# Kernel tuning notes

Measured on AMD Instinct MI355X. Metric: run time of the kernel, lower is better.

The kernel has to match this reference:

```python
import jax, jax.numpy as jnp
import numpy as np

N = 50000
E = 1600000
D_IN = 256
HID = 64
HEADS = 4


def setup_inputs() -> dict:
    key = jax.random.key(0)
    ks = jax.random.split(key, 8)
    x = jax.random.normal(ks[0], (N, D_IN), dtype=jnp.float32)
    edge_index = jax.random.randint(ks[1], (2, E), 0, N, dtype=jnp.int32)
    # GATConv params (PyG default: concat=True, negative_slope=0.2, add_self_loops=True)
    W = jax.random.normal(ks[2], (D_IN, HEADS * HID), dtype=jnp.float32) * (1.0 / np.sqrt(D_IN))
    att_src = jax.random.normal(ks[3], (HEADS, HID), dtype=jnp.float32) * 0.1
    att_dst = jax.random.normal(ks[4], (HEADS, HID), dtype=jnp.float32) * 0.1
    bias = jnp.zeros((HEADS * HID,), dtype=jnp.float32)
    # fc1: Linear(hidden*4, 3)
    fc1_W = jax.random.normal(ks[5], (HEADS * HID, 3), dtype=jnp.float32) * (1.0 / np.sqrt(HEADS * HID))
    fc1_b = jnp.zeros((3,), dtype=jnp.float32)
    return {"x": x, "edge_index": edge_index, "W": W, "att_src": att_src,
            "att_dst": att_dst, "bias": bias, "fc1_W": fc1_W, "fc1_b": fc1_b}


def _gat_conv(x, edge_index, W, att_src, att_dst, bias):
    n = x.shape[0]
    xp = (x @ W).reshape(n, HEADS, HID)  # [N,H,C]
    # add self loops (PyG default)
    loops = jnp.arange(n, dtype=edge_index.dtype)
    src = jnp.concatenate([edge_index[0], loops])  # [E+N]
    dst = jnp.concatenate([edge_index[1], loops])
    a_src = jnp.sum(xp * att_src, axis=-1)  # [N,H]
    a_dst = jnp.sum(xp * att_dst, axis=-1)
    alpha = jax.nn.leaky_relu(a_src[src] + a_dst[dst], negative_slope=0.2)  # [E+N,H]
    # segment softmax over incoming edges of each dst node
    amax = jax.ops.segment_max(alpha, dst, num_segments=n)
    ex = jnp.exp(alpha - amax[dst])
    denom = jax.ops.segment_sum(ex, dst, num_segments=n)
    alpha = ex / (denom[dst] + 1e-16)
    msg = xp[src] * alpha[:, :, None]  # [E+N,H,C]
    out = jax.ops.segment_sum(msg, dst, num_segments=n)  # [N,H,C]
    return out.reshape(n, HEADS * HID) + bias


def reference(x, edge_index, W, att_src, att_dst, bias, fc1_W, fc1_b):
    # dropout is identity at inference
    h = _gat_conv(x, edge_index, W, att_src, att_dst, bias)
    h = jax.nn.leaky_relu(h, negative_slope=0.01)  # F.leaky_relu default slope
    edge_rep = h[edge_index[0]] * h[edge_index[1]] * 0.5  # [E, H*HID]
    edge_scores = edge_rep @ fc1_W + fc1_b  # [E, 3]
    return edge_scores
```

## Files before the change

### kernel.cpp

```cpp
#include <hip/hip_runtime.h>
#include <hip/hip_fp16.h>
#include <math.h>

constexpr int N    = 50000;
constexpr int E    = 1600000;
constexpr int F    = 256;
constexpr int EL   = E + N;
constexpr int NBLK = (N + 255) / 256;

typedef _Float16 v8hf __attribute__((ext_vector_type(8)));
typedef float    v4f  __attribute__((ext_vector_type(4)));

__global__ void k_cvt_x(const float* __restrict__ x, _Float16* __restrict__ xh) {
  const size_t i = ((size_t)blockIdx.x * 256 + threadIdx.x) * 4;
  const float4 v = *(const float4*)(x + i);
  _Float16 h[4] = {(_Float16)v.x, (_Float16)v.y, (_Float16)v.z, (_Float16)v.w};
  *(uint2*)(xh + i) = *(const uint2*)h;
}

__global__ void k_cvt_w(const float* __restrict__ W, _Float16* __restrict__ wt) {
  const int id = blockIdx.x * 256 + threadIdx.x;
  const int n = id >> 8, k = id & 255;
  wt[id] = (_Float16)W[k * 256 + n];
}

__global__ void k_cvt_w3(const float* __restrict__ fc1W, _Float16* __restrict__ wt3h) {
  const int id = blockIdx.x * 256 + threadIdx.x;
  const int n = id >> 8, k = id & 255;
  wt3h[id] = (n < 3) ? (_Float16)(0.5f * fc1W[k * 3 + n]) : (_Float16)0.f;
}

__global__ __launch_bounds__(256) void k_xw_mfma(
    const _Float16* __restrict__ xh, const _Float16* __restrict__ wt,
    const float* __restrict__ att_src, const float* __restrict__ att_dst,
    __half* __restrict__ xp, float* __restrict__ a_src, float* __restrict__ a_dst) {
  const int wv   = threadIdx.x >> 6;
  const int lane = threadIdx.x & 63;
  const int q = lane >> 4, l16 = lane & 15;
  const int m0 = blockIdx.x * 16;
  const int c0 = wv * 64;

  v4f acc[4] = {{0,0,0,0},{0,0,0,0},{0,0,0,0},{0,0,0,0}};
  const _Float16* arow = xh + (size_t)(m0 + l16) * 256 + q * 8;
  const _Float16* brow = wt + (size_t)(c0 + l16) * 256 + q * 8;

  for (int kc = 0; kc < 256; kc += 32) {
    const v8hf a = *(const v8hf*)(arow + kc);
    #pragma unroll
    for (int tn = 0; tn < 4; ++tn) {
      const v8hf b = *(const v8hf*)(brow + (size_t)tn * 16 * 256 + kc);
      acc[tn] = __builtin_amdgcn_mfma_f32_16x16x32_f16(a, b, acc[tn], 0, 0, 0);
    }
  }

  #pragma unroll
  for (int tn = 0; tn < 4; ++tn) {
    const int col = c0 + tn * 16 + l16;
    #pragma unroll
    for (int r = 0; r < 4; ++r)
      xp[(size_t)(m0 + q * 4 + r) * 256 + col] = __float2half_rn(acc[tn][r]);
  }

  float aw[4], dw[4];
  #pragma unroll
  for (int tn = 0; tn < 4; ++tn) {
    aw[tn] = att_src[c0 + tn * 16 + l16];
    dw[tn] = att_dst[c0 + tn * 16 + l16];
  }
  #pragma unroll
  for (int r = 0; r < 4; ++r) {
    float ps = acc[0][r]*aw[0] + acc[1][r]*aw[1] + acc[2][r]*aw[2] + acc[3][r]*aw[3];
    float pd = acc[0][r]*dw[0] + acc[1][r]*dw[1] + acc[2][r]*dw[2] + acc[3][r]*dw[3];
    #pragma unroll
    for (int off = 1; off < 16; off <<= 1) {
      ps += __shfl_xor(ps, off, 16);
      pd += __shfl_xor(pd, off, 16);
    }
    if (l16 == 0) {
      a_src[(m0 + q * 4 + r) * 4 + wv] = ps;
      a_dst[(m0 + q * 4 + r) * 4 + wv] = pd;
    }
  }
}

__global__ void k_hist(const int* __restrict__ ei, int* __restrict__ counts) {
  const int i = blockIdx.x * blockDim.x + threadIdx.x;
  if (i < E) atomicAdd(&counts[ei[E + i]], 1);
}

__global__ __launch_bounds__(256) void k_scan1(
    const int* __restrict__ counts, int* __restrict__ offsets, int* __restrict__ partials) {
  __shared__ int s[256];
  const int t = threadIdx.x;
  const int i = blockIdx.x * 256 + t;
  const int v = (i < N) ? counts[i] + 1 : 0;
  s[t] = v;
  __syncthreads();
  for (int off = 1; off < 256; off <<= 1) {
    const int add = (t >= off) ? s[t - off] : 0;
    __syncthreads();
    s[t] += add;
    __syncthreads();
  }
  if (i < N) offsets[i] = s[t] - v;
  if (t == 255) partials[blockIdx.x] = s[255];
}

__global__ __launch_bounds__(256) void k_scan2(int* __restrict__ partials) {
  __shared__ int s[256];
  const int t = threadIdx.x;
  const int v = (t < NBLK) ? partials[t] : 0;
  s[t] = v;
  __syncthreads();
  for (int off = 1; off < 256; off <<= 1) {
    const int add = (t >= off) ? s[t - off] : 0;
    __syncthreads();
    s[t] += add;
    __syncthreads();
  }
  if (t < NBLK) partials[t] = s[t] - v;
}

__global__ void k_scan3(int* __restrict__ offsets, const int* __restrict__ partials,
                        int* __restrict__ cursor) {
  const int i = blockIdx.x * 256 + threadIdx.x;
  if (i < N) {
    const int v = offsets[i] + partials[blockIdx.x];
    offsets[i] = v;
    cursor[i]  = v;
  }
  if (i == 0) offsets[N] = EL;
}

__global__ void k_scatter(const int* __restrict__ ei, int* __restrict__ cursor,
                          int2* __restrict__ se) {
  const int i = blockIdx.x * blockDim.x + threadIdx.x;
  if (i >= EL) return;
  int s, d, id;
  if (i < E) { s = ei[i]; d = ei[E + i]; id = i; }
  else       { s = d = i - E; id = -1; }
  const int pos = atomicAdd(&cursor[d], 1);
  se[pos] = make_int2(s, id);
}

__global__ __launch_bounds__(128) void k_agg(
    const __half* __restrict__ xp, const float* __restrict__ a_src,
    const float* __restrict__ a_dst, const int2* __restrict__ se,
    const int* __restrict__ offsets, const float* __restrict__ bias,
    __half* __restrict__ h) {
  const int n = blockIdx.x * 2 + (threadIdx.x >> 6);
  const int lane = threadIdx.x & 63;
  const int hd = lane >> 4, es = lane & 15;
  const int beg = offsets[n], end = offsets[n + 1];
  const float adst = a_dst[n * 4 + hd];
  const __half* xb = xp + (size_t)lane * 4;

  float a0 = 0.f, a1 = 0.f, a2 = 0.f, a3 = 0.f, den = 0.f;

  for (int c = beg; c < end; c += 16) {
    const int cnt = min(16, end - c);
    int sv = 0; float wvv = 0.f;
    if (es < cnt) {
      sv = se[c + es].x;
      float al = a_src[sv * 4 + hd] + adst;
      al = al > 0.f ? al : 0.2f * al;
      wvv = __expf(al);
    }
    int j = 0;
    for (; j + 4 <= cnt; j += 4) {
      const int   s0 = __shfl(sv, j + 0, 16), s1 = __shfl(sv, j + 1, 16);
      const int   s2 = __shfl(sv, j + 2, 16), s3 = __shfl(sv, j + 3, 16);
      const float w0 = __shfl(wvv, j + 0, 16), w1 = __shfl(wvv, j + 1, 16);
      const float w2 = __shfl(wvv, j + 2, 16), w3 = __shfl(wvv, j + 3, 16);
      const uint2 r0 = *(const uint2*)(xb + (size_t)s0 * 256);
      const uint2 r1 = *(const uint2*)(xb + (size_t)s1 * 256);
      const uint2 r2 = *(const uint2*)(xb + (size_t)s2 * 256);
      const uint2 r3 = *(const uint2*)(xb + (size_t)s3 * 256);
      den += (w0 + w1) + (w2 + w3);
      {
        const __half2* p = (const __half2*)&r0;
        const float2 lo = __half22float2(p[0]), hi = __half22float2(p[1]);
        a0 += w0 * lo.x; a1 += w0 * lo.y; a2 += w0 * hi.x; a3 += w0 * hi.y;
      }
      {
        const __half2* p = (const __half2*)&r1;
        const float2 lo = __half22float2(p[0]), hi = __half22float2(p[1]);
        a0 += w1 * lo.x; a1 += w1 * lo.y; a2 += w1 * hi.x; a3 += w1 * hi.y;
      }
      {
        const __half2* p = (const __half2*)&r2;
        const float2 lo = __half22float2(p[0]), hi = __half22float2(p[1]);
        a0 += w2 * lo.x; a1 += w2 * lo.y; a2 += w2 * hi.x; a3 += w2 * hi.y;
      }
      {
        const __half2* p = (const __half2*)&r3;
        const float2 lo = __half22float2(p[0]), hi = __half22float2(p[1]);
        a0 += w3 * lo.x; a1 += w3 * lo.y; a2 += w3 * hi.x; a3 += w3 * hi.y;
      }
    }
    for (; j < cnt; ++j) {
      const int   s = __shfl(sv, j, 16);
      const float w = __shfl(wvv, j, 16);
      const uint2 r = *(const uint2*)(xb + (size_t)s * 256);
      const __half2* p = (const __half2*)&r;
      const float2 lo = __half22float2(p[0]), hi = __half22float2(p[1]);
      den += w;
      a0 += w * lo.x; a1 += w * lo.y; a2 += w * hi.x; a3 += w * hi.y;
    }
  }

  const float inv = 1.f / (den + 1e-16f);
  const float4 bv = *(const float4*)(bias + lane * 4);
  float o0 = a0 * inv + bv.x, o1 = a1 * inv + bv.y;
  float o2 = a2 * inv + bv.z, o3 = a3 * inv + bv.w;
  o0 = o0 > 0.f ? o0 : 0.01f * o0;
  o1 = o1 > 0.f ? o1 : 0.01f * o1;
  o2 = o2 > 0.f ? o2 : 0.01f * o2;
  o3 = o3 > 0.f ? o3 : 0.01f * o3;
  const __half2 p0 = __floats2half2_rn(o0, o1), p1 = __floats2half2_rn(o2, o3);
  uint2 st;
  st.x = *(const unsigned*)&p0;
  st.y = *(const unsigned*)&p1;
  *(uint2*)(h + (size_t)n * 256 + lane * 4) = st;
}

__global__ __launch_bounds__(256) void k_score_mfma(
    const _Float16* __restrict__ h, const int2* __restrict__ se,
    const int* __restrict__ offsets, const _Float16* __restrict__ wt3h,
    const float* __restrict__ fc1b, float* __restrict__ out) {
  const int n = blockIdx.x * 4 + (threadIdx.x >> 6);
  const int lane = threadIdx.x & 63;
  const int q = lane >> 4, l16 = lane & 15;

  v8hf bfrag[8];
  {
    const _Float16* brow = wt3h + l16 * 256 + q * 8;
    #pragma unroll
    for (int kci = 0; kci < 8; ++kci)
      bfrag[kci] = *(const v8hf*)(brow + kci * 32);
  }
  v8hf hdv[8];
  {
    const _Float16* drow = h + (size_t)n * 256 + q * 8;
    #pragma unroll
    for (int kci = 0; kci < 8; ++kci)
      hdv[kci] = *(const v8hf*)(drow + kci * 32);
  }
  const float bn = (l16 < 3) ? fc1b[l16] : 0.f;

  const int beg = offsets[n], end = offsets[n + 1];
  for (int c = beg; c < end; c += 16) {
    const int idx = c + l16;
    int s = -1, eid = -1;
    if (idx < end) { const int2 p = se[idx]; s = p.x; eid = p.y; }

    v8hf av[8] = {};
    if (s >= 0) {
      const _Float16* srow = h + (size_t)s * 256 + q * 8;
      #pragma unroll
      for (int kci = 0; kci < 8; ++kci)
        av[kci] = *(const v8hf*)(srow + kci * 32);
    }

    v4f acc = {0.f, 0.f, 0.f, 0.f};
    #pragma unroll
    for (int kci = 0; kci < 8; ++kci) {
      const v8hf ar = av[kci] * hdv[kci];
      acc = __builtin_amdgcn_mfma_f32_16x16x32_f16(ar, bfrag[kci], acc, 0, 0, 0);
    }

    #pragma unroll
    for (int r = 0; r < 4; ++r) {
      const int m = q * 4 + r;
      const int em = __shfl(eid, m, 16);
      if (l16 < 3 && c + m < end && em >= 0)
        out[(size_t)em * 3 + l16] = acc[r] + bn;
    }
  }
}

static inline size_t align256(size_t b) { return (b + 255) & ~(size_t)255; }

extern "C" void kernel_launch(void* const* d_in, const int* in_sizes, int n_in,
                              void* d_out, int out_size, void* d_ws, size_t ws_size,
                              hipStream_t stream) {
  const float* x    = (const float*)d_in[0];
  const int*   ei   = (const int*)  d_in[1];
  const float* W    = (const float*)d_in[2];
  const float* attS = (const float*)d_in[3];
  const float* attD = (const float*)d_in[4];
  const float* bias = (const float*)d_in[5];
  const float* fc1W = (const float*)d_in[6];
  const float* fc1b = (const float*)d_in[7];
  float*       out  = (float*)d_out;
  char*        ws   = (char*)d_ws;

  size_t off = 0;
  auto alloc = [&](size_t bytes) -> void* {
    void* p = ws + off;
    off += align256(bytes);
    return p;
  };
  _Float16* xh     = (_Float16*)alloc((size_t)N * F * sizeof(_Float16));
  _Float16* wt     = (_Float16*)alloc((size_t)F * F * sizeof(_Float16));
  _Float16* wt3h   = (_Float16*)alloc((size_t)16 * F * sizeof(_Float16));
  __half*   xp     = (__half*)  alloc((size_t)N * F * sizeof(__half));
  __half*   hbuf   = (__half*)  alloc((size_t)N * F * sizeof(__half));
  float*    a_src  = (float*)   alloc((size_t)N * 4 * sizeof(float));
  float*    a_dst  = (float*)   alloc((size_t)N * 4 * sizeof(float));
  int*      counts = (int*)     alloc((size_t)N * sizeof(int));
  int*      offs   = (int*)     alloc((size_t)(N + 1) * sizeof(int));
  int*      partial= (int*)     alloc(256 * sizeof(int));
  int*      cursor = (int*)     alloc((size_t)N * sizeof(int));
  int2*     se     = (int2*)    alloc((size_t)EL * sizeof(int2));

  hipMemsetAsync(counts, 0, (size_t)N * sizeof(int), stream);

  k_cvt_x<<<(N * F / 4 + 255) / 256, 256, 0, stream>>>(x, xh);
  k_cvt_w<<<F * F / 256, 256, 0, stream>>>(W, wt);
  k_cvt_w3<<<16, 256, 0, stream>>>(fc1W, wt3h);
  k_xw_mfma<<<N / 16, 256, 0, stream>>>(xh, wt, attS, attD, xp, a_src, a_dst);
  k_hist<<<(E + 255) / 256, 256, 0, stream>>>(ei, counts);
  k_scan1<<<NBLK, 256, 0, stream>>>(counts, offs, partial);
  k_scan2<<<1, 256, 0, stream>>>(partial);
  k_scan3<<<NBLK, 256, 0, stream>>>(offs, partial, cursor);
  k_scatter<<<(EL + 255) / 256, 256, 0, stream>>>(ei, cursor, se);
  k_agg<<<N / 2, 128, 0, stream>>>(xp, a_src, a_dst, se, offs, bias, hbuf);
  k_score_mfma<<<(N + 3) / 4, 256, 0, stream>>>((const _Float16*)hbuf, se, offs,
                                                wt3h, fc1b, out);
}
```

Before: 665.0 us.

## Fuse prep kernels, fold x conversion and histogram into GEMM, flatten scoring

The separate x, W and fc1 conversion kernels and the memset are merged into one prep kernel. The fp32 x is now converted to half inside the MFMA GEMM, and the degree histogram runs as a tail loop of that GEMM. The scan's second and third passes are merged. Aggregation now uses two waves per node, each taking alternating 16-edge chunks, with the partial sums reduced through shared memory. Scoring becomes a flat grid-stride loop over 16-edge chunks and reads the destination index from a widened int4 CSR entry. The aim is fewer launches, no materialised half copy of x, and better load balance for high-degree nodes, at the cost of doubling the CSR size and redundant dst-row gathers in scoring.

```diff
diff --git a/kernel.cpp b/kernel.cpp
--- a/kernel.cpp
+++ b/kernel.cpp
@@ -7,32 +7,31 @@
 constexpr int F    = 256;
 constexpr int EL   = E + N;
 constexpr int NBLK = (N + 255) / 256;
+constexpr int CH   = (EL + 15) / 16;
 
 typedef _Float16 v8hf __attribute__((ext_vector_type(8)));
 typedef float    v4f  __attribute__((ext_vector_type(4)));
 
-__global__ void k_cvt_x(const float* __restrict__ x, _Float16* __restrict__ xh) {
-  const size_t i = ((size_t)blockIdx.x * 256 + threadIdx.x) * 4;
-  const float4 v = *(const float4*)(x + i);
-  _Float16 h[4] = {(_Float16)v.x, (_Float16)v.y, (_Float16)v.z, (_Float16)v.w};
-  *(uint2*)(xh + i) = *(const uint2*)h;
-}
-
-__global__ void k_cvt_w(const float* __restrict__ W, _Float16* __restrict__ wt) {
-  const int id = blockIdx.x * 256 + threadIdx.x;
-  const int n = id >> 8, k = id & 255;
-  wt[id] = (_Float16)W[k * 256 + n];
-}
-
-__global__ void k_cvt_w3(const float* __restrict__ fc1W, _Float16* __restrict__ wt3h) {
-  const int id = blockIdx.x * 256 + threadIdx.x;
-  const int n = id >> 8, k = id & 255;
-  wt3h[id] = (n < 3) ? (_Float16)(0.5f * fc1W[k * 3 + n]) : (_Float16)0.f;
+__global__ __launch_bounds__(256) void k_prep(
+    const float* __restrict__ W, const float* __restrict__ fc1W,
+    _Float16* __restrict__ wt, _Float16* __restrict__ wt3h,
+    int* __restrict__ counts) {
+  const int t = blockIdx.x * 256 + threadIdx.x;
+  {
+    const int n = t >> 8, k = t & 255;
+    wt[t] = (_Float16)W[k * 256 + n];
+  }
+  if (t < 4096) {
+    const int n = t >> 8, k = t & 255;
+    wt3h[t] = (n < 3) ? (_Float16)(0.5f * fc1W[k * 3 + n]) : (_Float16)0.f;
+  }
+  if (t < N) counts[t] = 0;
 }
 
 __global__ __launch_bounds__(256) void k_xw_mfma(
-    const _Float16* __restrict__ xh, const _Float16* __restrict__ wt,
+    const float* __restrict__ x, const _Float16* __restrict__ wt,
     const float* __restrict__ att_src, const float* __restrict__ att_dst,
+    const int* __restrict__ ei, int* __restrict__ counts,
     __half* __restrict__ xp, float* __restrict__ a_src, float* __restrict__ a_dst) {
   const int wv   = threadIdx.x >> 6;
   const int lane = threadIdx.x & 63;
@@ -41,11 +40,14 @@
   const int c0 = wv * 64;
 
   v4f acc[4] = {{0,0,0,0},{0,0,0,0},{0,0,0,0},{0,0,0,0}};
-  const _Float16* arow = xh + (size_t)(m0 + l16) * 256 + q * 8;
+  const float*    arow = x  + (size_t)(m0 + l16) * 256 + q * 8;
   const _Float16* brow = wt + (size_t)(c0 + l16) * 256 + q * 8;
 
   for (int kc = 0; kc < 256; kc += 32) {
-    const v8hf a = *(const v8hf*)(arow + kc);
+    const float4 f0 = *(const float4*)(arow + kc);
+    const float4 f1 = *(const float4*)(arow + kc + 4);
+    const v8hf a = {(_Float16)f0.x, (_Float16)f0.y, (_Float16)f0.z, (_Float16)f0.w,
+                    (_Float16)f1.x, (_Float16)f1.y, (_Float16)f1.z, (_Float16)f1.w};
     #pragma unroll
     for (int tn = 0; tn < 4; ++tn) {
       const v8hf b = *(const v8hf*)(brow + (size_t)tn * 16 * 256 + kc);
@@ -81,11 +83,9 @@
       a_dst[(m0 + q * 4 + r) * 4 + wv] = pd;
     }
   }
-}
-
-__global__ void k_hist(const int* __restrict__ ei, int* __restrict__ counts) {
-  const int i = blockIdx.x * blockDim.x + threadIdx.x;
-  if (i < E) atomicAdd(&counts[ei[E + i]], 1);
+
+  const int gid = blockIdx.x * 256 + threadIdx.x;
+  for (int i = gid; i < E; i += 800000) atomicAdd(&counts[ei[E + i]], 1);
 }
 
 __global__ __launch_bounds__(256) void k_scan1(
@@ -106,9 +106,11 @@
   if (t == 255) partials[blockIdx.x] = s[255];
 }
 
-__global__ __launch_bounds__(256) void k_scan2(int* __restrict__ partials) {
+__global__ __launch_bounds__(256) void k_scan3b(
+    int* __restrict__ offsets, const int* __restrict__ partials,
+    int* __restrict__ cursor) {
   __shared__ int s[256];
-  const int t = threadIdx.x;
+  const int t = threadIdx.x, b = blockIdx.x;
   const int v = (t < NBLK) ? partials[t] : 0;
   s[t] = v;
   __syncthreads();
@@ -118,38 +120,35 @@
     s[t] += add;
     __syncthreads();
   }
-  if (t < NBLK) partials[t] = s[t] - v;
-}
-
-__global__ void k_scan3(int* __restrict__ offsets, const int* __restrict__ partials,
-                        int* __restrict__ cursor) {
-  const int i = blockIdx.x * 256 + threadIdx.x;
+  const int pre = (b == 0) ? 0 : s[b - 1];
+  const int i = b * 256 + t;
   if (i < N) {
-    const int v = offsets[i] + partials[blockIdx.x];
-    offsets[i] = v;
-    cursor[i]  = v;
+    const int val = offsets[i] + pre;
+    offsets[i] = val;
+    cursor[i]  = val;
   }
   if (i == 0) offsets[N] = EL;
 }
 
 __global__ void k_scatter(const int* __restrict__ ei, int* __restrict__ cursor,
-                          int2* __restrict__ se) {
+                          int4* __restrict__ se) {
   const int i = blockIdx.x * blockDim.x + threadIdx.x;
   if (i >= EL) return;
   int s, d, id;
   if (i < E) { s = ei[i]; d = ei[E + i]; id = i; }
   else       { s = d = i - E; id = -1; }
   const int pos = atomicAdd(&cursor[d], 1);
-  se[pos] = make_int2(s, id);
+  se[pos] = make_int4(s, id, d, 0);
 }
 
 __global__ __launch_bounds__(128) void k_agg(
     const __half* __restrict__ xp, const float* __restrict__ a_src,
-    const float* __restrict__ a_dst, const int2* __restrict__ se,
+    const float* __restrict__ a_dst, const int4* __restrict__ se,
     const int* __restrict__ offsets, const float* __restrict__ bias,
     __half* __restrict__ h) {
-  const int n = blockIdx.x * 2 + (threadIdx.x >> 6);
-  const int lane = threadIdx.x & 63;
+  const int n = blockIdx.x;
+  const int t = threadIdx.x;
+  const int wv = t >> 6, lane = t & 63;
   const int hd = lane >> 4, es = lane & 15;
   const int beg = offsets[n], end = offsets[n + 1];
   const float adst = a_dst[n * 4 + hd];
@@ -157,7 +156,7 @@
 
   float a0 = 0.f, a1 = 0.f, a2 = 0.f, a3 = 0.f, den = 0.f;
 
-  for (int c = beg; c < end; c += 16) {
+  for (int c = beg + wv * 16; c < end; c += 32) {
     const int cnt = min(16, end - c);
     int sv = 0; float wvv = 0.f;
     if (es < cnt) {
@@ -166,106 +165,100 @@
       al = al > 0.f ? al : 0.2f * al;
       wvv = __expf(al);
     }
-    int j = 0;
-    for (; j + 4 <= cnt; j += 4) {
-      const int   s0 = __shfl(sv, j + 0, 16), s1 = __shfl(sv, j + 1, 16);
-      const int   s2 = __shfl(sv, j + 2, 16), s3 = __shfl(sv, j + 3, 16);
-      const float w0 = __shfl(wvv, j + 0, 16), w1 = __shfl(wvv, j + 1, 16);
-      const float w2 = __shfl(wvv, j + 2, 16), w3 = __shfl(wvv, j + 3, 16);
-      const uint2 r0 = *(const uint2*)(xb + (size_t)s0 * 256);
-      const uint2 r1 = *(const uint2*)(xb + (size_t)s1 * 256);
-      const uint2 r2 = *(const uint2*)(xb + (size_t)s2 * 256);
-      const uint2 r3 = *(const uint2*)(xb + (size_t)s3 * 256);
-      den += (w0 + w1) + (w2 + w3);
-      {
-        const __half2* p = (const __half2*)&r0;
+    if (cnt == 16) {
+      #pragma unroll
+      for (int g = 0; g < 2; ++g) {
+        int ss[8]; float ww[8]; uint2 rr[8];
+        #pragma unroll
+        for (int j = 0; j < 8; ++j) {
+          ss[j] = __shfl(sv,  g * 8 + j, 16);
+          ww[j] = __shfl(wvv, g * 8 + j, 16);
+        }
+        #pragma unroll
+        for (int j = 0; j < 8; ++j) rr[j] = *(const uint2*)(xb + (size_t)ss[j] * 256);
+        #pragma unroll
+        for (int j = 0; j < 8; ++j) {
+          const __half2* p = (const __half2*)&rr[j];
+          const float2 lo = __half22float2(p[0]), hi = __half22float2(p[1]);
+          den += ww[j];
+          a0 += ww[j] * lo.x; a1 += ww[j] * lo.y;
+          a2 += ww[j] * hi.x; a3 += ww[j] * hi.y;
+        }
+      }
+    } else {
+      for (int j = 0; j < cnt; ++j) {
+        const int   s = __shfl(sv, j, 16);
+        const float w = __shfl(wvv, j, 16);
+        const uint2 r = *(const uint2*)(xb + (size_t)s * 256);
+        const __half2* p = (const __half2*)&r;
         const float2 lo = __half22float2(p[0]), hi = __half22float2(p[1]);
-        a0 += w0 * lo.x; a1 += w0 * lo.y; a2 += w0 * hi.x; a3 += w0 * hi.y;
+        den += w;
+        a0 += w * lo.x; a1 += w * lo.y; a2 += w * hi.x; a3 += w * hi.y;
       }
-      {
-        const __half2* p = (const __half2*)&r1;
-        const float2 lo = __half22float2(p[0]), hi = __half22float2(p[1]);
-        a0 += w1 * lo.x; a1 += w1 * lo.y; a2 += w1 * hi.x; a3 += w1 * hi.y;
-      }
-      {
-        const __half2* p = (const __half2*)&r2;
-        const float2 lo = __half22float2(p[0]), hi = __half22float2(p[1]);
-        a0 += w2 * lo.x; a1 += w2 * lo.y; a2 += w2 * hi.x; a3 += w2 * hi.y;
-      }
-      {
-        const __half2* p = (const __half2*)&r3;
-        const float2 lo = __half22float2(p[0]), hi = __half22float2(p[1]);
-        a0 += w3 * lo.x; a1 += w3 * lo.y; a2 += w3 * hi.x; a3 += w3 * hi.y;
-      }
-    }
-    for (; j < cnt; ++j) {
-      const int   s = __shfl(sv, j, 16);
-      const float w = __shfl(wvv, j, 16);
-      const uint2 r = *(const uint2*)(xb + (size_t)s * 256);
-      const __half2* p = (const __half2*)&r;
-      const float2 lo = __half22float2(p[0]), hi = __half22float2(p[1]);
-      den += w;
-      a0 += w * lo.x; a1 += w * lo.y; a2 += w * hi.x; a3 += w * hi.y;
-    }
-  }
-
-  const float inv = 1.f / (den + 1e-16f);
-  const float4 bv = *(const float4*)(bias + lane * 4);
-  float o0 = a0 * inv + bv.x, o1 = a1 * inv + bv.y;
-  float o2 = a2 * inv + bv.z, o3 = a3 * inv + bv.w;
-  o0 = o0 > 0.f ? o0 : 0.01f * o0;
-  o1 = o1 > 0.f ? o1 : 0.01f * o1;
-  o2 = o2 > 0.f ? o2 : 0.01f * o2;
-  o3 = o3 > 0.f ? o3 : 0.01f * o3;
-  const __half2 p0 = __floats2half2_rn(o0, o1), p1 = __floats2half2_rn(o2, o3);
-  uint2 st;
-  st.x = *(const unsigned*)&p0;
-  st.y = *(const unsigned*)&p1;
-  *(uint2*)(h + (size_t)n * 256 + lane * 4) = st;
-}
-
-__global__ __launch_bounds__(256) void k_score_mfma(
-    const _Float16* __restrict__ h, const int2* __restrict__ se,
-    const int* __restrict__ offsets, const _Float16* __restrict__ wt3h,
-    const float* __restrict__ fc1b, float* __restrict__ out) {
-  const int n = blockIdx.x * 4 + (threadIdx.x >> 6);
+    }
+  }
+
+  __shared__ float ra[256];
+  __shared__ float rd[64];
+  if (wv == 1) {
+    ra[lane * 4 + 0] = a0; ra[lane * 4 + 1] = a1;
+    ra[lane * 4 + 2] = a2; ra[lane * 4 + 3] = a3;
+    rd[lane] = den;
+  }
+  __syncthreads();
+  if (wv == 0) {
+    a0 += ra[lane * 4 + 0]; a1 += ra[lane * 4 + 1];
+    a2 += ra[lane * 4 + 2]; a3 += ra[lane * 4 + 3];
+    den += rd[lane];
+    const float inv = 1.f / (den + 1e-16f);
+    const float4 bv = *(const float4*)(bias + lane * 4);
+    float o0 = a0 * inv + bv.x, o1 = a1 * inv + bv.y;
+    float o2 = a2 * inv + bv.z, o3 = a3 * inv + bv.w;
+    o0 = o0 > 0.f ? o0 : 0.01f * o0;
+    o1 = o1 > 0.f ? o1 : 0.01f * o1;
+    o2 = o2 > 0.f ? o2 : 0.01f * o2;
+    o3 = o3 > 0.f ? o3 : 0.01f * o3;
+    const __half2 p0 = __floats2half2_rn(o0, o1), p1 = __floats2half2_rn(o2, o3);
+    uint2 st;
+    st.x = *(const unsigned*)&p0;
+    st.y = *(const unsigned*)&p1;
+    *(uint2*)(h + (size_t)n * 256 + lane * 4) = st;
+  }
+}
+
+__global__ __launch_bounds__(256) void k_score_flat(
+    const _Float16* __restrict__ h, const int4* __restrict__ se,
+    const _Float16* __restrict__ wt3h, const float* __restrict__ fc1b,
+    float* __restrict__ out, int total_waves) {
   const int lane = threadIdx.x & 63;
   const int q = lane >> 4, l16 = lane & 15;
+  const int wgid = blockIdx.x * 4 + (threadIdx.x >> 6);
 
   v8hf bfrag[8];
   {
     const _Float16* brow = wt3h + l16 * 256 + q * 8;
     #pragma unroll
-    for (int kci = 0; kci < 8; ++kci)
-      bfrag[kci] = *(const v8hf*)(brow + kci * 32);
-  }
-  v8hf hdv[8];
-  {
-    const _Float16* drow = h + (size_t)n * 256 + q * 8;
-    #pragma unroll
-    for (int kci = 0; kci < 8; ++kci)
-      hdv[kci] = *(const v8hf*)(drow + kci * 32);
+    for (int kci = 0; kci < 8; ++kci) bfrag[kci] = *(const v8hf*)(brow + kci * 32);
   }
   const float bn = (l16 < 3) ? fc1b[l16] : 0.f;
 
-  const int beg = offsets[n], end = offsets[n + 1];
-  for (int c = beg; c < end; c += 16) {
-    const int idx = c + l16;
-    int s = -1, eid = -1;
-    if (idx < end) { const int2 p = se[idx]; s = p.x; eid = p.y; }
-
-    v8hf av[8] = {};
-    if (s >= 0) {
-      const _Float16* srow = h + (size_t)s * 256 + q * 8;
-      #pragma unroll
-      for (int kci = 0; kci < 8; ++kci)
-        av[kci] = *(const v8hf*)(srow + kci * 32);
-    }
+  for (int ch = wgid; ch < CH; ch += total_waves) {
+    const int idx = ch * 16 + l16;
+    int s = 0, d = 0, eid = -1;
+    if (idx < EL) { const int4 p = se[idx]; s = p.x; eid = p.y; d = p.z; }
+
+    const _Float16* srow = h + (size_t)s * 256 + q * 8;
+    const _Float16* drow = h + (size_t)d * 256 + q * 8;
+    v8hf av[8], dv[8];
+    #pragma unroll
+    for (int kci = 0; kci < 8; ++kci) av[kci] = *(const v8hf*)(srow + kci * 32);
+    #pragma unroll
+    for (int kci = 0; kci < 8; ++kci) dv[kci] = *(const v8hf*)(drow + kci * 32);
 
     v4f acc = {0.f, 0.f, 0.f, 0.f};
     #pragma unroll
     for (int kci = 0; kci < 8; ++kci) {
-      const v8hf ar = av[kci] * hdv[kci];
+      const v8hf ar = av[kci] * dv[kci];
       acc = __builtin_amdgcn_mfma_f32_16x16x32_f16(ar, bfrag[kci], acc, 0, 0, 0);
     }
 
@@ -273,7 +266,7 @@
     for (int r = 0; r < 4; ++r) {
       const int m = q * 4 + r;
       const int em = __shfl(eid, m, 16);
-      if (l16 < 3 && c + m < end && em >= 0)
+      if (l16 < 3 && em >= 0)
         out[(size_t)em * 3 + l16] = acc[r] + bn;
     }
   }
@@ -301,7 +294,6 @@
     off += align256(bytes);
     return p;
   };
-  _Float16* xh     = (_Float16*)alloc((size_t)N * F * sizeof(_Float16));
   _Float16* wt     = (_Float16*)alloc((size_t)F * F * sizeof(_Float16));
   _Float16* wt3h   = (_Float16*)alloc((size_t)16 * F * sizeof(_Float16));
   __half*   xp     = (__half*)  alloc((size_t)N * F * sizeof(__half));
@@ -312,20 +304,16 @@
   int*      offs   = (int*)     alloc((size_t)(N + 1) * sizeof(int));
   int*      partial= (int*)     alloc(256 * sizeof(int));
   int*      cursor = (int*)     alloc((size_t)N * sizeof(int));
-  int2*     se     = (int2*)    alloc((size_t)EL * sizeof(int2));
-
-  hipMemsetAsync(counts, 0, (size_t)N * sizeof(int), stream);
-
-  k_cvt_x<<<(N * F / 4 + 255) / 256, 256, 0, stream>>>(x, xh);
-  k_cvt_w<<<F * F / 256, 256, 0, stream>>>(W, wt);
-  k_cvt_w3<<<16, 256, 0, stream>>>(fc1W, wt3h);
-  k_xw_mfma<<<N / 16, 256, 0, stream>>>(xh, wt, attS, attD, xp, a_src, a_dst);
-  k_hist<<<(E + 255) / 256, 256, 0, stream>>>(ei, counts);
+  int4*     se     = (int4*)    alloc((size_t)EL * sizeof(int4));
+
+  k_prep<<<256, 256, 0, stream>>>(W, fc1W, wt, wt3h, counts);
+  k_xw_mfma<<<N / 16, 256, 0, stream>>>(x, wt, attS, attD, ei, counts,
+                                        xp, a_src, a_dst);
   k_scan1<<<NBLK, 256, 0, stream>>>(counts, offs, partial);
-  k_scan2<<<1, 256, 0, stream>>>(partial);
-  k_scan3<<<NBLK, 256, 0, stream>>>(offs, partial, cursor);
+  k_scan3b<<<NBLK, 256, 0, stream>>>(offs, partial, cursor);
   k_scatter<<<(EL + 255) / 256, 256, 0, stream>>>(ei, cursor, se);
-  k_agg<<<N / 2, 128, 0, stream>>>(xp, a_src, a_dst, se, offs, bias, hbuf);
-  k_score_mfma<<<(N + 3) / 4, 256, 0, stream>>>((const _Float16*)hbuf, se, offs,
-                                                wt3h, fc1b, out);
-}
+  k_agg<<<N, 128, 0, stream>>>(xp, a_src, a_dst, se, offs, bias, hbuf);
+  const int score_blocks = 4096;
+  k_score_flat<<<score_blocks, 256, 0, stream>>>((const _Float16*)hbuf, se, wt3h,
+                                                 fc1b, out, score_blocks * 4);
+}
```

Result: faster. 594.7 us (-10.6%).
